# Performance work log

Measured on AMD Instinct MI355X. Metric: run time of the kernel, lower is better.

Reference implementation:

```python
import jax, jax.numpy as jnp
import numpy as np

T, B = 128, 512
IN = 512          # input_size = prod(observation_shape)
H = 1024          # hidden size
NA = 256          # n_actions
IDX0 = jnp.arange(0, 128)    # sub_indices[0]
IDX1 = jnp.arange(128, 256)  # sub_indices[1]


def _mlp(x, w1, b1, w2, b2, w3, b3):
    h = jnp.tanh(x @ w1.T + b1)
    h = jnp.tanh(h @ w2.T + b2)
    return h @ w3.T + b3


def _linear_init(key, out_dim, in_dim):
    kw, kb = jax.random.split(key)
    s = 1.0 / np.sqrt(in_dim)
    w = jax.random.uniform(kw, (out_dim, in_dim), jnp.float32, -s, s)
    b = jax.random.uniform(kb, (out_dim,), jnp.float32, -s, s)
    return w, b


def setup_inputs() -> dict:
    key = jax.random.key(0)
    ks = jax.random.split(key, 12)
    # observation: [T,B,IN+3]; last 3 dims are the routing gate features
    core = jax.random.normal(ks[0], (T, B, IN), jnp.float32)
    gate = jax.random.uniform(ks[1], (T, B, 3), jnp.float32, -0.2, 0.2)
    obs = jnp.concatenate([core, gate], axis=-1)
    pf_w1, pf_b1 = _linear_init(ks[2], H, IN)
    pf_w2, pf_b2 = _linear_init(ks[3], H, H)
    pf_w3, pf_b3 = _linear_init(ks[4], 128, H)
    pc_w1, pc_b1 = _linear_init(ks[5], H, IN)
    pc_w2, pc_b2 = _linear_init(ks[6], H, H)
    pc_w3, pc_b3 = _linear_init(ks[7], 128, H)
    v_w1, v_b1 = _linear_init(ks[8], H, IN)
    v_w2, v_b2 = _linear_init(ks[9], H, H)
    v_w3, v_b3 = _linear_init(ks[10], 1, H)
    return dict(
        observation=obs,
        prev_action=jnp.zeros((T, B), jnp.int32),
        prev_reward=jnp.zeros((T, B), jnp.float32),
        pf_w1=pf_w1, pf_b1=pf_b1, pf_w2=pf_w2, pf_b2=pf_b2, pf_w3=pf_w3, pf_b3=pf_b3,
        pc_w1=pc_w1, pc_b1=pc_b1, pc_w2=pc_w2, pc_b2=pc_b2, pc_w3=pc_w3, pc_b3=pc_b3,
        v_w1=v_w1, v_b1=v_b1, v_w2=v_w2, v_b2=v_b2, v_w3=v_w3, v_b3=v_b3,
    )


def reference(observation, prev_action, prev_reward,
              pf_w1, pf_b1, pf_w2, pf_b2, pf_w3, pf_b3,
              pc_w1, pc_b1, pc_w2, pc_b2, pc_w3, pc_b3,
              v_w1, v_b1, v_w2, v_b2, v_w3, v_b3):
    obs_flat = observation.reshape(T * B, -1)      # [TB, IN+3]
    x = obs_flat[:, :IN]                            # [TB, IN]
    # routing: free expert iff all 3 gate features have |.| <= 0.1
    mask = jnp.all(jnp.abs(obs_flat[:, IN:IN + 3]) <= 0.1, axis=-1)  # [TB]
    p_free = jax.nn.softmax(_mlp(x, pf_w1, pf_b1, pf_w2, pf_b2, pf_w3, pf_b3), axis=-1)
    p_con = jax.nn.softmax(_mlp(x, pc_w1, pc_b1, pc_w2, pc_b2, pc_w3, pc_b3), axis=-1)
    zeros = jnp.zeros((T * B, NA), x.dtype)
    pi_free = zeros.at[:, IDX0].set(p_free)
    pi_con = zeros.at[:, IDX1].set(p_con)
    pi = jnp.where(mask[:, None], pi_free, pi_con)  # [TB, NA]
    v = _mlp(x, v_w1, v_b1, v_w2, v_b2, v_w3, v_b3).squeeze(-1)  # [TB]
    return pi.reshape(T, B, NA), v.reshape(T, B)
```

## Files before the change

kernel.cpp:

```cpp
#include <hip/hip_runtime.h>
#include <stdint.h>

#define M_TOTAL 65536
#define IN_DIM 512
#define OBS_DIM 515

typedef __bf16 bf16x8 __attribute__((ext_vector_type(8)));
typedef float f32x4 __attribute__((ext_vector_type(4)));
typedef unsigned short u16x8 __attribute__((ext_vector_type(8)));

__device__ __forceinline__ unsigned short f2bf(float f) {
  unsigned u = __float_as_uint(f);
  u = (u + 0x7FFFu + ((u >> 16) & 1u)) >> 16;
  return (unsigned short)u;
}
__device__ __forceinline__ float bf2f(unsigned short h) {
  return __uint_as_float(((unsigned)h) << 16);
}
__device__ __forceinline__ float fast_tanh(float z) {
  float e = __expf(2.0f * z);
  return 1.0f - 2.0f / (e + 1.0f);
}
__device__ __forceinline__ void gl16(const void* g, void* l) {
  __builtin_amdgcn_global_load_lds(
      (__attribute__((address_space(1))) void*)g,
      (__attribute__((address_space(3))) void*)l, 16, 0, 0);
}

struct P8 { const float* p[8]; };

__global__ __launch_bounds__(256) void fused_cast(
    P8 srcs, unsigned short* __restrict__ dst, int* __restrict__ cnt) {
  if (blockIdx.x == 0 && threadIdx.x < 128) cnt[threadIdx.x] = 0;
  const int b0 = 524288, b1 = 1048576, b2 = 1572864, b3 = 2621440,
            b4 = 3670016, b5 = 4718592, b6 = 4849664, b7 = 4980736;
  int stride = gridDim.x * 256;
  for (int i = blockIdx.x * 256 + threadIdx.x; i < b7; i += stride) {
    const float* s; int off;
    if (i < b2)      { if (i < b0) { s = srcs.p[0]; off = i; }
                       else if (i < b1) { s = srcs.p[1]; off = i - b0; }
                       else { s = srcs.p[2]; off = i - b1; } }
    else if (i < b5) { if (i < b3) { s = srcs.p[3]; off = i - b2; }
                       else if (i < b4) { s = srcs.p[4]; off = i - b3; }
                       else { s = srcs.p[5]; off = i - b4; } }
    else             { if (i < b6) { s = srcs.p[6]; off = i - b5; }
                       else { s = srcs.p[7]; off = i - b6; } }
    dst[i] = f2bf(s[off]);
  }
}

__global__ __launch_bounds__(256) void compact_kernel(
    const float* __restrict__ obs,
    int* __restrict__ cntF, int* __restrict__ cntC,
    int* __restrict__ idxF, int* __restrict__ idxC, int C) {
  __shared__ int lcF, lcC, baseF, baseC;
  const int tid = threadIdx.x;
  const int r = blockIdx.x * 256 + tid;
  const float* g = obs + (size_t)r * OBS_DIM + IN_DIM;
  bool m = (fabsf(g[0]) <= 0.1f) && (fabsf(g[1]) <= 0.1f) && (fabsf(g[2]) <= 0.1f);
  if (tid == 0) { lcF = 0; lcC = 0; }
  __syncthreads();
  int slot = m ? atomicAdd(&lcF, 1) : atomicAdd(&lcC, 1);
  __syncthreads();
  const int c = r / C;
  if (tid == 0) {
    baseF = atomicAdd(&cntF[c], lcF);
    baseC = atomicAdd(&cntC[c], lcC);
  }
  __syncthreads();
  const int local = r - c * C;
  if (m) idxF[(size_t)c * C + baseF + slot] = local;
  else   idxC[(size_t)c * C + baseC + slot] = local;
}

__global__ __launch_bounds__(256) void build_idxP(
    const int* __restrict__ cntF, const int* __restrict__ cntC,
    const int* __restrict__ idxF, const int* __restrict__ idxC,
    int* __restrict__ idxP, int* __restrict__ meta, int C, int Cp) {
  const int bpc = Cp >> 8;
  const int c = blockIdx.x / bpc;
  const int i = (blockIdx.x % bpc) * 256 + threadIdx.x;
  const int cf = cntF[c], cc = cntC[c];
  const int padF = (cf + 255) & ~255;
  const int total = padF + ((cc + 255) & ~255);
  if ((blockIdx.x % bpc) == 0 && threadIdx.x == 0) {
    meta[2 * c] = padF; meta[2 * c + 1] = total;
  }
  if (i >= total) return;
  int v;
  if (i < padF) v = idxF[(size_t)c * C + (i < cf ? i : 0)];
  else { int j = i - padF; v = idxC[(size_t)c * C + (j < cc ? j : 0)]; }
  idxP[(size_t)c * Cp + i] = v;
}

__global__ __launch_bounds__(256) void prep_x(
    const float* __restrict__ obs, unsigned short* __restrict__ x, int row0) {
  int g = blockIdx.x * 256 + threadIdx.x;
  int row = g >> 9, col = g & 511;
  x[g] = f2bf(obs[(size_t)(row0 + row) * OBS_DIM + col]);
}

#define STAGE_A(h, tt, db) { \
    const unsigned short* _s = pA[h] + (size_t)(tt) * 64 + grp8; \
    char* _d = smem + (db) * 65536 + (h) * 16384 + wbase; \
    gl16(_s, _d); gl16(_s + 32, _d + 8192); }
#define STAGE_B(h, tt, db) { \
    const unsigned short* _s = pB[h] + (size_t)(tt) * 64 + grp8; \
    char* _d = smem + (db) * 65536 + 32768 + (h) * 16384 + wbase; \
    gl16(_s, _d); gl16(_s + 32, _d + 8192); }

__global__ __launch_bounds__(512) void gemm256(
    const unsigned short* __restrict__ A, int lda,
    const unsigned short* __restrict__ BF, const unsigned short* __restrict__ BC,
    const float* __restrict__ biasF, const float* __restrict__ biasC,
    unsigned short* __restrict__ Cmat, int ldc, int K,
    const int* __restrict__ idxP, const int* __restrict__ meta, int Mrows)
{
  extern __shared__ char smem[];
  const int tid = threadIdx.x;

  const int nwg = gridDim.x * gridDim.y;
  const int orig = blockIdx.y * gridDim.x + blockIdx.x;
  const int qq = nwg >> 3, rr = nwg & 7, xc = orig & 7, oo = orig >> 3;
  const int wg = (xc < rr ? xc * (qq + 1) : rr * (qq + 1) + (xc - rr) * qq) + oo;
  const int n0 = (wg % gridDim.x) << 8;
  const int m0 = (wg / gridDim.x) << 8;

  const int padF  = meta ? meta[0] : (1 << 30);
  const int total = meta ? meta[1] : Mrows;
  if (m0 >= total) return;
  const unsigned short* B = (m0 < padF) ? BF : BC;
  const float* bias = (m0 < padF) ? biasF : biasC;

  const int lane = tid & 63;
  const int wv = tid >> 6;
  const int wm = wv >> 2, wn = wv & 3;
  const int lr = lane & 15;
  const int lk = lane >> 4;

  const int srow = tid >> 2;
  const int grp8 = (((tid & 3) ^ ((srow >> 1) & 3)) << 3);
  const int wbase = (tid & ~63) << 4;
  const unsigned short* pA[2];
  const unsigned short* pB[2];
#pragma unroll
  for (int h = 0; h < 2; ++h) {
    int gr = m0 + h * 128 + srow;
    int ga = idxP ? idxP[gr] : gr;
    pA[h] = A + (size_t)ga * lda;
    pB[h] = B + (size_t)(n0 + h * 128 + srow) * K;
  }

  int a_off[4], b_off[2];
#pragma unroll
  for (int f = 0; f < 4; ++f) {
    int hr = wm * 64 + f * 16 + lr;
    a_off[f] = hr * 64 + ((lk ^ ((hr >> 1) & 3)) << 4);
  }
#pragma unroll
  for (int g = 0; g < 2; ++g) {
    int hb = wn * 32 + g * 16 + lr;
    b_off[g] = hb * 64 + ((lk ^ ((hb >> 1) & 3)) << 4);
  }

  const f32x4 zero = {0.f, 0.f, 0.f, 0.f};
  f32x4 acc[8][4];
#pragma unroll
  for (int i = 0; i < 8; ++i)
#pragma unroll
    for (int j = 0; j < 4; ++j) acc[i][j] = zero;

  const int NT = K >> 6;
  STAGE_A(0, 0, 0); STAGE_B(0, 0, 0); STAGE_A(1, 0, 0); STAGE_B(1, 0, 0);
  STAGE_A(0, 1, 1); STAGE_B(0, 1, 1);
  asm volatile("s_waitcnt vmcnt(4)" ::: "memory");
  __builtin_amdgcn_s_barrier();

  bf16x8 a[4][2], b0[2][2], b1[2][2];
  for (int T = 0; T < NT; ++T) {
    const int b = T & 1;
    const int tt1 = (T + 1 < NT) ? T + 1 : NT - 1;
    const int tt2 = (T + 2 < NT) ? T + 2 : NT - 1;
#pragma unroll
    for (int q = 0; q < 4; ++q) {
      const int mh = q >> 1, nh = q & 1;
      if (q == 0) {
        const char* Ab = smem + b * 65536;
        const char* Bb = smem + b * 65536 + 32768;
#pragma unroll
        for (int f = 0; f < 4; ++f)
#pragma unroll
          for (int kk = 0; kk < 2; ++kk)
            a[f][kk] = *(const bf16x8*)(Ab + kk * 8192 + a_off[f]);
#pragma unroll
        for (int g = 0; g < 2; ++g)
#pragma unroll
          for (int kk = 0; kk < 2; ++kk)
            b0[g][kk] = *(const bf16x8*)(Bb + kk * 8192 + b_off[g]);
      } else if (q == 1) {
        const char* Bb = smem + b * 65536 + 32768 + 16384;
#pragma unroll
        for (int g = 0; g < 2; ++g)
#pragma unroll
          for (int kk = 0; kk < 2; ++kk)
            b1[g][kk] = *(const bf16x8*)(Bb + kk * 8192 + b_off[g]);
      } else if (q == 2) {
        const char* Ab = smem + b * 65536 + 16384;
#pragma unroll
        for (int f = 0; f < 4; ++f)
#pragma unroll
          for (int kk = 0; kk < 2; ++kk)
            a[f][kk] = *(const bf16x8*)(Ab + kk * 8192 + a_off[f]);
      }
      if (q == 0)      { STAGE_A(1, tt1, b ^ 1); }
      else if (q == 1) { STAGE_B(1, tt1, b ^ 1); }
      else if (q == 2) { STAGE_A(0, tt2, b); }
      else             { STAGE_B(0, tt2, b); }
      __builtin_amdgcn_s_barrier();
      asm volatile("s_waitcnt lgkmcnt(0)" ::: "memory");
      __builtin_amdgcn_sched_barrier(0);
      __builtin_amdgcn_s_setprio(1);
#pragma unroll
      for (int f = 0; f < 4; ++f)
#pragma unroll
        for (int g = 0; g < 2; ++g)
#pragma unroll
          for (int kk = 0; kk < 2; ++kk) {
            if (nh == 0)
              acc[mh * 4 + f][g] = __builtin_amdgcn_mfma_f32_16x16x32_bf16(
                  a[f][kk], b0[g][kk], acc[mh * 4 + f][g], 0, 0, 0);
            else
              acc[mh * 4 + f][2 + g] = __builtin_amdgcn_mfma_f32_16x16x32_bf16(
                  a[f][kk], b1[g][kk], acc[mh * 4 + f][2 + g], 0, 0, 0);
          }
      __builtin_amdgcn_s_setprio(0);
      if (q == 3) asm volatile("s_waitcnt vmcnt(4)" ::: "memory");
      __builtin_amdgcn_s_barrier();
    }
  }

#pragma unroll
  for (int N = 0; N < 4; ++N) {
    const int nh = N >> 1, g = N & 1;
    int col = n0 + nh * 128 + wn * 32 + g * 16 + lr;
    float bv = bias[col];
#pragma unroll
    for (int M = 0; M < 8; ++M) {
      const int mh = M >> 2, f = M & 3;
      int rowb = m0 + mh * 128 + wm * 64 + f * 16 + lk * 4;
#pragma unroll
      for (int r = 0; r < 4; ++r)
        Cmat[(size_t)(rowb + r) * ldc + col] = f2bf(fast_tanh(acc[M][N][r] + bv));
    }
  }
}

__global__ __launch_bounds__(256) void l3_policy_p(
    const unsigned short* __restrict__ H2,
    const unsigned short* __restrict__ W3F, const unsigned short* __restrict__ W3C,
    const float* __restrict__ b3F, const float* __restrict__ b3C,
    const int* __restrict__ idxP, const int* __restrict__ meta,
    float* __restrict__ out_pi, int row0)
{
  __shared__ alignas(16) unsigned short sA[128 * 32];
  __shared__ alignas(16) unsigned short sB[128 * 32];
  __shared__ int s_idx[128];
  const int tid = threadIdx.x;
  const int m0 = blockIdx.x << 7;
  const int padF = meta[0], total = meta[1];
  if (m0 >= total) return;
  const bool freeg = (m0 < padF);
  const unsigned short* W3 = freeg ? W3F : W3C;
  const float* b3 = freeg ? b3F : b3C;
  const int half = freeg ? 0 : 128;
  if (tid < 128) s_idx[tid] = idxP[m0 + tid];
  __syncthreads();

  const int lane = tid & 63;
  const int wv = tid >> 6;
  const int lr = lane & 15;
  const int lk = lane >> 4;

  const int ar0 = tid >> 2, ar1 = (256 + tid) >> 2;
  const int acol = (tid & 3) << 3;
  const unsigned short* Ap0 = H2 + (size_t)(m0 + ar0) * 1024 + acol;
  const unsigned short* Ap1 = H2 + (size_t)(m0 + ar1) * 1024 + acol;
  const unsigned short* Bp0 = W3 + (size_t)ar0 * 1024 + acol;
  const unsigned short* Bp1 = W3 + (size_t)ar1 * 1024 + acol;
  const int du = (tid & ~63) << 3;

  const f32x4 zero = {0.f, 0.f, 0.f, 0.f};
  f32x4 acc[2][8];
#pragma unroll
  for (int i = 0; i < 2; ++i)
#pragma unroll
    for (int j = 0; j < 8; ++j) acc[i][j] = zero;

  for (int kt = 0; kt < 1024; kt += 32) {
    __syncthreads();
    gl16(Ap0 + kt, &sA[du]);
    gl16(Bp0 + kt, &sB[du]);
    gl16(Ap1 + kt, &sA[du + 2048]);
    gl16(Bp1 + kt, &sB[du + 2048]);
    __syncthreads();
    bf16x8 af[2], bfr[8];
#pragma unroll
    for (int i = 0; i < 2; ++i)
      af[i] = *(const bf16x8*)&sA[((wv << 5) + (i << 4) + lr) * 32 + (lk << 3)];
#pragma unroll
    for (int j = 0; j < 8; ++j)
      bfr[j] = *(const bf16x8*)&sB[((j << 4) + lr) * 32 + (lk << 3)];
#pragma unroll
    for (int i = 0; i < 2; ++i)
#pragma unroll
      for (int j = 0; j < 8; ++j)
        acc[i][j] = __builtin_amdgcn_mfma_f32_16x16x32_bf16(af[i], bfr[j], acc[i][j], 0, 0, 0);
  }

  float bv[8];
#pragma unroll
  for (int j = 0; j < 8; ++j) bv[j] = b3[(j << 4) + lr];

#pragma unroll
  for (int i = 0; i < 2; ++i) {
#pragma unroll
    for (int r = 0; r < 4; ++r) {
      float lg[8];
      float mx = -3.4e38f;
#pragma unroll
      for (int j = 0; j < 8; ++j) { lg[j] = acc[i][j][r] + bv[j]; mx = fmaxf(mx, lg[j]); }
#pragma unroll
      for (int d = 1; d < 16; d <<= 1) mx = fmaxf(mx, __shfl_xor(mx, d));
      float s = 0.f;
#pragma unroll
      for (int j = 0; j < 8; ++j) { lg[j] = __expf(lg[j] - mx); s += lg[j]; }
#pragma unroll
      for (int d = 1; d < 16; d <<= 1) s += __shfl_xor(s, d);
      float inv = 1.f / s;
      int compact = m0 + (wv << 5) + (i << 4) + (lk << 2) + r;
      int grow = row0 + s_idx[compact - m0];
      size_t base = (size_t)grow * 256;
#pragma unroll
      for (int j = 0; j < 8; ++j)
        out_pi[base + half + (j << 4) + lr] = lg[j] * inv;
#pragma unroll
      for (int j = 0; j < 8; ++j)
        out_pi[base + (half ^ 128) + (j << 4) + lr] = 0.0f;
    }
  }
}

__global__ __launch_bounds__(256) void l3_value(
    const unsigned short* __restrict__ H2,
    const float* __restrict__ w3,
    const float* __restrict__ b3,
    float* __restrict__ out_v, int row0, int C)
{
  const int lane = threadIdx.x & 63;
  const int row = (blockIdx.x << 2) + (threadIdx.x >> 6);
  if (row >= C) return;
  float s = 0.f;
#pragma unroll
  for (int it = 0; it < 2; ++it) {
    int k = (it << 9) + (lane << 3);
    u16x8 h = *(const u16x8*)(H2 + (size_t)row * 1024 + k);
    const float4* wp = (const float4*)(w3 + k);
    float4 w0 = wp[0], w1 = wp[1];
    s += bf2f(h[0]) * w0.x + bf2f(h[1]) * w0.y + bf2f(h[2]) * w0.z + bf2f(h[3]) * w0.w;
    s += bf2f(h[4]) * w1.x + bf2f(h[5]) * w1.y + bf2f(h[6]) * w1.z + bf2f(h[7]) * w1.w;
  }
#pragma unroll
  for (int d = 1; d < 64; d <<= 1) s += __shfl_xor(s, d);
  if (lane == 0) out_v[row0 + row] = s + b3[0];
}

extern "C" void kernel_launch(void* const* d_in, const int* in_sizes, int n_in,
                              void* d_out, int out_size, void* d_ws, size_t ws_size,
                              hipStream_t stream)
{
  (void)in_sizes; (void)n_in; (void)out_size;
  const float* obs   = (const float*)d_in[0];
  const float* pf_w1 = (const float*)d_in[3];
  const float* pf_b1 = (const float*)d_in[4];
  const float* pf_w2 = (const float*)d_in[5];
  const float* pf_b2 = (const float*)d_in[6];
  const float* pf_w3 = (const float*)d_in[7];
  const float* pf_b3 = (const float*)d_in[8];
  const float* pc_w1 = (const float*)d_in[9];
  const float* pc_b1 = (const float*)d_in[10];
  const float* pc_w2 = (const float*)d_in[11];
  const float* pc_b2 = (const float*)d_in[12];
  const float* pc_w3 = (const float*)d_in[13];
  const float* pc_b3 = (const float*)d_in[14];
  const float* v_w1  = (const float*)d_in[15];
  const float* v_b1  = (const float*)d_in[16];
  const float* v_w2  = (const float*)d_in[17];
  const float* v_b2  = (const float*)d_in[18];
  const float* v_w3  = (const float*)d_in[19];
  const float* v_b3  = (const float*)d_in[20];

  float* out_pi = (float*)d_out;
  float* out_v  = out_pi + (size_t)M_TOTAL * 256;

  char* ws = (char*)d_ws;
  unsigned short* wPF1 = (unsigned short*)ws;
  unsigned short* wPC1 = wPF1 + 524288;
  unsigned short* wV1  = wPC1 + 524288;
  unsigned short* wPF2 = wV1  + 524288;
  unsigned short* wPC2 = wPF2 + 1048576;
  unsigned short* wV2  = wPC2 + 1048576;
  unsigned short* wPF3 = wV2  + 1048576;
  unsigned short* wPC3 = wPF3 + 131072;
  int* cntF = (int*)(wPC3 + 131072);
  int* cntC = cntF + 64;
  int* idxF = cntC + 64;
  int* idxC = idxF + 65536;
  int* meta = idxC + 65536;
  int* idxP = meta + 128;
  unsigned short* xb = (unsigned short*)(idxP + 81920);

  const size_t fixed = (size_t)9961472 + 4 * (64 + 64 + 65536 + 65536 + 128 + 81920);
  int C = 1024;
  if      (ws_size >= fixed + 5120ull * 65536 + 3145728) C = 65536;
  else if (ws_size >= fixed + 5120ull * 32768 + 3145728) C = 32768;
  else if (ws_size >= fixed + 5120ull * 16384 + 3145728) C = 16384;
  else if (ws_size >= fixed + 5120ull *  8192 + 3145728) C = 8192;
  else if (ws_size >= fixed + 5120ull *  4096 + 3145728) C = 4096;
  else if (ws_size >= fixed + 5120ull *  2048 + 3145728) C = 2048;
  const int nchunk = M_TOTAL / C;
  const int Cp = C + 512;

  unsigned short* h1p = xb + (size_t)C * 512;
  unsigned short* h2p = h1p + (size_t)Cp * 1024;

  (void)hipFuncSetAttribute((const void*)gemm256,
      hipFuncAttributeMaxDynamicSharedMemorySize, 131072);

  P8 srcs;
  srcs.p[0] = pf_w1; srcs.p[1] = pc_w1; srcs.p[2] = v_w1;
  srcs.p[3] = pf_w2; srcs.p[4] = pc_w2; srcs.p[5] = v_w2;
  srcs.p[6] = pf_w3; srcs.p[7] = pc_w3;
  fused_cast<<<2048, 256, 0, stream>>>(srcs, wPF1, cntF);
  compact_kernel<<<M_TOTAL / 256, 256, 0, stream>>>(obs, cntF, cntC, idxF, idxC, C);
  build_idxP<<<nchunk * (Cp / 256), 256, 0, stream>>>(cntF, cntC, idxF, idxC, idxP, meta, C, Cp);

  const dim3 gv(4, C / 256);
  const dim3 gp(4, Cp / 256);
  for (int c = 0; c < nchunk; ++c) {
    int row0 = c * C;
    prep_x<<<C * 512 / 256, 256, 0, stream>>>(obs, xb, row0);
    gemm256<<<gv, 512, 131072, stream>>>(xb, 512, wV1, wV1, v_b1, v_b1,
                                         h1p, 1024, 512, nullptr, nullptr, C);
    gemm256<<<gv, 512, 131072, stream>>>(h1p, 1024, wV2, wV2, v_b2, v_b2,
                                         h2p, 1024, 1024, nullptr, nullptr, C);
    l3_value<<<C / 4, 256, 0, stream>>>(h2p, v_w3, v_b3, out_v, row0, C);
    gemm256<<<gp, 512, 131072, stream>>>(xb, 512, wPF1, wPC1, pf_b1, pc_b1,
                                         h1p, 1024, 512, idxP + (size_t)c * Cp, meta + 2 * c, 0);
    gemm256<<<gp, 512, 131072, stream>>>(h1p, 1024, wPF2, wPC2, pf_b2, pc_b2,
                                         h2p, 1024, 1024, nullptr, meta + 2 * c, 0);
    l3_policy_p<<<Cp / 128, 256, 0, stream>>>(h2p, wPF3, wPC3, pf_b3, pc_b3,
                                              idxP + (size_t)c * Cp, meta + 2 * c, out_pi, row0);
  }
}
```

Before: 725.9 us.

## Software-pipeline LDS fragment reads ahead of MFMA phases in gemm256

Restructures the K loop so each quarter-phase issues the LDS reads for the next phase (double-buffered A fragments, separate B1 registers) before running the current MFMAs, dropping the explicit lgkmcnt(0) wait in front of each MFMA block. Redundant clamped prefetches on the last tiles are skipped, with a full vmcnt drain at the tail. It also sets launch_bounds(512,2) to request two workgroups per CU. The added fragment registers raise register pressure, and the occupancy hint could cause spills; LDS usage may still limit occupancy anyway.

Result: faster. 702.2 us (median of 2 runs) (-3.3%).

```diff
diff --git a/kernel.cpp b/kernel.cpp
--- a/kernel.cpp
+++ b/kernel.cpp
@@ -108,8 +108,26 @@
     const unsigned short* _s = pB[h] + (size_t)(tt) * 64 + grp8; \
     char* _d = smem + (db) * 65536 + 32768 + (h) * 16384 + wbase; \
     gl16(_s, _d); gl16(_s + 32, _d + 8192); }
-
-__global__ __launch_bounds__(512) void gemm256(
+#define RD_A(dst, base) \
+  _Pragma("unroll") for (int _f = 0; _f < 4; ++_f) \
+  _Pragma("unroll") for (int _k = 0; _k < 2; ++_k) \
+    dst[_f][_k] = *(const bf16x8*)((base) + _k * 8192 + a_off[_f]);
+#define RD_B(dst, base) \
+  _Pragma("unroll") for (int _g = 0; _g < 2; ++_g) \
+  _Pragma("unroll") for (int _k = 0; _k < 2; ++_k) \
+    dst[_g][_k] = *(const bf16x8*)((base) + _k * 8192 + b_off[_g]);
+#define MFMA16(AF, BFR, MB, NB) \
+  _Pragma("unroll") for (int _f = 0; _f < 4; ++_f) \
+  _Pragma("unroll") for (int _g = 0; _g < 2; ++_g) \
+  _Pragma("unroll") for (int _k = 0; _k < 2; ++_k) \
+    acc[(MB) + _f][(NB) + _g] = __builtin_amdgcn_mfma_f32_16x16x32_bf16( \
+        AF[_f][_k], BFR[_g][_k], acc[(MB) + _f][(NB) + _g], 0, 0, 0);
+#define PH_TAIL() \
+  asm volatile("" ::: "memory"); \
+  __builtin_amdgcn_s_barrier(); \
+  __builtin_amdgcn_sched_barrier(0);
+
+__global__ __launch_bounds__(512, 2) void gemm256(
     const unsigned short* __restrict__ A, int lda,
     const unsigned short* __restrict__ BF, const unsigned short* __restrict__ BC,
     const float* __restrict__ biasF, const float* __restrict__ biasC,
@@ -171,72 +189,58 @@
     for (int j = 0; j < 4; ++j) acc[i][j] = zero;
 
   const int NT = K >> 6;
+
   STAGE_A(0, 0, 0); STAGE_B(0, 0, 0); STAGE_A(1, 0, 0); STAGE_B(1, 0, 0);
   STAGE_A(0, 1, 1); STAGE_B(0, 1, 1);
   asm volatile("s_waitcnt vmcnt(4)" ::: "memory");
   __builtin_amdgcn_s_barrier();
-
-  bf16x8 a[4][2], b0[2][2], b1[2][2];
+  asm volatile("" ::: "memory");
+
+  bf16x8 aA[4][2], aB[4][2], b0[2][2], rb1[2][2];
+  RD_A(aA, smem);
+  RD_B(b0, smem + 32768);
+
   for (int T = 0; T < NT; ++T) {
     const int b = T & 1;
-    const int tt1 = (T + 1 < NT) ? T + 1 : NT - 1;
-    const int tt2 = (T + 2 < NT) ? T + 2 : NT - 1;
-#pragma unroll
-    for (int q = 0; q < 4; ++q) {
-      const int mh = q >> 1, nh = q & 1;
-      if (q == 0) {
-        const char* Ab = smem + b * 65536;
-        const char* Bb = smem + b * 65536 + 32768;
-#pragma unroll
-        for (int f = 0; f < 4; ++f)
-#pragma unroll
-          for (int kk = 0; kk < 2; ++kk)
-            a[f][kk] = *(const bf16x8*)(Ab + kk * 8192 + a_off[f]);
-#pragma unroll
-        for (int g = 0; g < 2; ++g)
-#pragma unroll
-          for (int kk = 0; kk < 2; ++kk)
-            b0[g][kk] = *(const bf16x8*)(Bb + kk * 8192 + b_off[g]);
-      } else if (q == 1) {
-        const char* Bb = smem + b * 65536 + 32768 + 16384;
-#pragma unroll
-        for (int g = 0; g < 2; ++g)
-#pragma unroll
-          for (int kk = 0; kk < 2; ++kk)
-            b1[g][kk] = *(const bf16x8*)(Bb + kk * 8192 + b_off[g]);
-      } else if (q == 2) {
-        const char* Ab = smem + b * 65536 + 16384;
-#pragma unroll
-        for (int f = 0; f < 4; ++f)
-#pragma unroll
-          for (int kk = 0; kk < 2; ++kk)
-            a[f][kk] = *(const bf16x8*)(Ab + kk * 8192 + a_off[f]);
-      }
-      if (q == 0)      { STAGE_A(1, tt1, b ^ 1); }
-      else if (q == 1) { STAGE_B(1, tt1, b ^ 1); }
-      else if (q == 2) { STAGE_A(0, tt2, b); }
-      else             { STAGE_B(0, tt2, b); }
-      __builtin_amdgcn_s_barrier();
-      asm volatile("s_waitcnt lgkmcnt(0)" ::: "memory");
-      __builtin_amdgcn_sched_barrier(0);
-      __builtin_amdgcn_s_setprio(1);
-#pragma unroll
-      for (int f = 0; f < 4; ++f)
-#pragma unroll
-        for (int g = 0; g < 2; ++g)
-#pragma unroll
-          for (int kk = 0; kk < 2; ++kk) {
-            if (nh == 0)
-              acc[mh * 4 + f][g] = __builtin_amdgcn_mfma_f32_16x16x32_bf16(
-                  a[f][kk], b0[g][kk], acc[mh * 4 + f][g], 0, 0, 0);
-            else
-              acc[mh * 4 + f][2 + g] = __builtin_amdgcn_mfma_f32_16x16x32_bf16(
-                  a[f][kk], b1[g][kk], acc[mh * 4 + f][2 + g], 0, 0, 0);
-          }
-      __builtin_amdgcn_s_setprio(0);
-      if (q == 3) asm volatile("s_waitcnt vmcnt(4)" ::: "memory");
-      __builtin_amdgcn_s_barrier();
-    }
+    char* bufc = smem + (b << 16);
+    char* bufn = smem + ((b ^ 1) << 16);
+    const bool s1 = (T + 1 < NT);
+    const bool s2 = (T + 2 < NT);
+
+    RD_B(rb1, bufc + 49152);
+    if (s1) { STAGE_A(1, T + 1, b ^ 1); }
+    __builtin_amdgcn_sched_barrier(0);
+    __builtin_amdgcn_s_setprio(1);
+    MFMA16(aA, b0, 0, 0);
+    __builtin_amdgcn_s_setprio(0);
+    PH_TAIL();
+
+    RD_A(aB, bufc + 16384);
+    if (s1) { STAGE_B(1, T + 1, b ^ 1); }
+    __builtin_amdgcn_sched_barrier(0);
+    __builtin_amdgcn_s_setprio(1);
+    MFMA16(aA, rb1, 0, 2);
+    __builtin_amdgcn_s_setprio(0);
+    PH_TAIL();
+
+    if (s2) { STAGE_A(0, T + 2, b); }
+    __builtin_amdgcn_sched_barrier(0);
+    __builtin_amdgcn_s_setprio(1);
+    MFMA16(aB, b0, 4, 0);
+    __builtin_amdgcn_s_setprio(0);
+    if (s2) asm volatile("s_waitcnt vmcnt(4)" ::: "memory");
+    else    asm volatile("s_waitcnt vmcnt(0)" ::: "memory");
+    PH_TAIL();
+
+    if (s1) { RD_A(aA, bufn); RD_B(b0, bufn + 32768); }
+    if (s2) { STAGE_B(0, T + 2, b); }
+    __builtin_amdgcn_sched_barrier(0);
+    __builtin_amdgcn_s_setprio(1);
+    MFMA16(aB, rb1, 4, 2);
+    __builtin_amdgcn_s_setprio(0);
+    if (s2) asm volatile("s_waitcnt vmcnt(4)" ::: "memory");
+    else    asm volatile("s_waitcnt vmcnt(0)" ::: "memory");
+    PH_TAIL();
   }
 
 #pragma unroll
```
